# Kernel optimization log

Hardware: AMD Instinct MI355X
Metric: run time of the kernel (lower is better)

Reference implementation:

```python
import jax, jax.numpy as jnp
import numpy as np

BATCH = 256
SIZE = 512      # must be a power of two for the bitonic network
K = 16          # top-k
STEEPNESS = 10.0  # cauchy distribution scale (module default)


def _bitonic_layers(n):
    """Static index pairs of the bitonic sorting network (ascending).
    Returns (lefts, rights), each int32 [n_layers, n//2]. After a compare-swap,
    the soft-min goes to `left` and the soft-max goes to `right`."""
    lefts, rights = [], []
    k = 2
    while k <= n:
        j = k // 2
        while j >= 1:
            l_idx, r_idx = [], []
            for i in range(n):
                l = i ^ j
                if l > i:
                    if (i & k) == 0:   # ascending block: min at i
                        l_idx.append(i); r_idx.append(l)
                    else:              # descending block: min at l
                        l_idx.append(l); r_idx.append(i)
            lefts.append(l_idx); rights.append(r_idx)
            j //= 2
        k *= 2
    return np.asarray(lefts, np.int32), np.asarray(rights, np.int32)


def setup_inputs() -> dict:
    key = jax.random.key(0)
    vectors = jax.random.normal(key, (BATCH, SIZE), dtype=jnp.float32)
    return {"vectors": vectors}


def reference(vectors):
    b, n = vectors.shape
    lefts_np, rights_np = _bitonic_layers(n)
    lefts = jnp.asarray(lefts_np)
    rights = jnp.asarray(rights_np)
    # soft permutation matrix: X[b, i, j] = P(input j ends at sorted pos i)
    X0 = jnp.broadcast_to(jnp.eye(n, dtype=vectors.dtype)[None], (b, n, n))

    def step(carry, lr):
        x, X = carry
        l, r = lr                      # [n//2] index pairs for this layer
        a = x[:, l]                    # [b, n//2]
        c = x[:, r]
        # cauchy CDF of steepness*(c - a): prob that no swap is needed
        alpha = jnp.arctan((c - a) * STEEPNESS) / jnp.pi + 0.5
        x = x.at[:, l].set(alpha * a + (1.0 - alpha) * c)
        x = x.at[:, r].set(alpha * c + (1.0 - alpha) * a)
        Xl = X[:, l, :]                # [b, n//2, n]
        Xr = X[:, r, :]
        al = alpha[..., None]
        X = X.at[:, l, :].set(al * Xl + (1.0 - al) * Xr)
        X = X.at[:, r, :].set(al * Xr + (1.0 - al) * Xl)
        return (x, X), None

    (_, X), _ = jax.lax.scan(step, (vectors, X0), (lefts, rights))
    # ascending sort -> last K rows correspond to the K largest elements;
    # flip so row 0 = largest. Output: [batch, K, n] soft top-k distribution.
    return jnp.flip(X[:, n - K:, :], axis=1)
```

## Files before the change

### kernel.cpp

```cpp
#include <hip/hip_runtime.h>
#include <math.h>

#define N 512
#define BATCH 256
#define KTOP 16
#define NLAYERS 45
#define NPAIRS 256

template<int CTRL>
__device__ __forceinline__ float dpp_xor(float x) {
    return __int_as_float(
        __builtin_amdgcn_mov_dpp(__float_as_int(x), CTRL, 0xF, 0xF, true));
}

__device__ __forceinline__ float fast_alpha(float t) {
    const float at  = __builtin_fabsf(t);
    const bool inv  = at > 1.0f;
    const float z   = inv ? __builtin_amdgcn_rcpf(at) : at;
    const float s   = z * z;
    float p = -0.0117212f;
    p = __builtin_fmaf(p, s,  0.05265332f);
    p = __builtin_fmaf(p, s, -0.11643287f);
    p = __builtin_fmaf(p, s,  0.19354346f);
    p = __builtin_fmaf(p, s, -0.33262347f);
    p = __builtin_fmaf(p, s,  0.99997726f);
    float r = z * p;
    r = inv ? (1.5707963267948966f - r) : r;
    r = (t < 0.0f) ? -r : r;
    return __builtin_fmaf(r, 0.3183098861837907f, 0.5f);
}

__global__ __launch_bounds__(1024, 1)
void difftopk_kernel(const float* __restrict__ x_in, float* __restrict__ out) {
    __shared__ float xs[2][N];
    __shared__ __align__(16) float As[NLAYERS][NPAIRS];

    const int b    = blockIdx.x;
    const int tid  = threadIdx.x;
    const int lane = tid & 63;

    if (tid < N) {
        const int e = tid;
        float o = x_in[(size_t)b * N + e];

        int t = 0, par = 0;
        #pragma unroll
        for (int s = 1; s <= 9; ++s) {
            const int k  = 1 << s;
            const bool kb = (e & k) == 0;
            #pragma unroll
            for (int lg = s - 1; lg >= 0; --lg, ++t) {
                const int j = 1 << lg;
                float p;
                if (lg >= 6) {
                    xs[par][e] = o;
                    __syncthreads();
                    p = xs[par][e ^ j];
                    par ^= 1;
                } else if (lg == 0) {
                    p = dpp_xor<0xB1>(o);
                } else if (lg == 1) {
                    p = dpp_xor<0x4E>(o);
                } else if (lg == 3) {
                    p = dpp_xor<0x128>(o);
                } else {
                    p = __shfl_xor(o, j, 64);
                }
                const bool jb = (e & j) == 0;
                const float d = (kb == jb) ? (p - o) : (o - p);
                const float alpha = fast_alpha(d * 10.0f);
                o = __builtin_fmaf(alpha, o - p, p);
                if (jb) {
                    const int ord = ((e >> (lg + 1)) << lg) | (e & (j - 1));
                    As[t][ord] = alpha;
                }
            }
        }
        __syncthreads();
    } else {
        #pragma unroll 1
        for (int i = 0; i < 7; ++i) __syncthreads();
    }

    const int wave  = tid >> 6;
    const int lane8 = lane << 3;
    const int r     = N - 1 - wave;

    float v[8];
    #pragma unroll
    for (int m = 0; m < 8; ++m) v[m] = (lane8 + m == r) ? 1.0f : 0.0f;

    #pragma unroll
    for (int s = 9; s >= 1; --s) {
        const int base = (s * (s - 1)) >> 1;
        #pragma unroll
        for (int lg = 0; lg < s; ++lg) {
            const int tt = base + (s - 1 - lg);
            if (lg >= 3) {
                const int j    = 1 << lg;
                const int ordb = ((lane8 >> (lg + 1)) << lg) | (lane8 & (j - 1));
                const float4 a0 = *(const float4*)&As[tt][ordb];
                const float4 a1 = *(const float4*)&As[tt][ordb + 4];
                const float al[8] = {a0.x, a0.y, a0.z, a0.w, a1.x, a1.y, a1.z, a1.w};
                #pragma unroll
                for (int m = 0; m < 8; ++m) {
                    float p;
                    if (lg == 3)      p = dpp_xor<0xB1>(v[m]);
                    else if (lg == 4) p = dpp_xor<0x4E>(v[m]);
                    else if (lg == 6) p = dpp_xor<0x128>(v[m]);
                    else              p = __shfl_xor(v[m], j >> 3, 64);
                    v[m] = __builtin_fmaf(al[m], v[m] - p, p);
                }
            } else {
                const float4 a = *(const float4*)&As[tt][lane << 2];
                const float aa[4] = {a.x, a.y, a.z, a.w};
                if (lg == 2) {
                    #pragma unroll
                    for (int i = 0; i < 4; ++i) {
                        const float x0 = v[i], x1 = v[i + 4], d = x0 - x1;
                        v[i]     = __builtin_fmaf(aa[i],  d, x1);
                        v[i + 4] = __builtin_fmaf(aa[i], -d, x0);
                    }
                } else if (lg == 1) {
                    #pragma unroll
                    for (int i = 0; i < 4; ++i) {
                        const int lo = (((i >> 1) << 2) | (i & 1));
                        const float x0 = v[lo], x1 = v[lo + 2], d = x0 - x1;
                        v[lo]     = __builtin_fmaf(aa[i],  d, x1);
                        v[lo + 2] = __builtin_fmaf(aa[i], -d, x0);
                    }
                } else {
                    #pragma unroll
                    for (int i = 0; i < 4; ++i) {
                        const int lo = i << 1;
                        const float x0 = v[lo], x1 = v[lo + 1], d = x0 - x1;
                        v[lo]     = __builtin_fmaf(aa[i],  d, x1);
                        v[lo + 1] = __builtin_fmaf(aa[i], -d, x0);
                    }
                }
            }
        }
    }

    float4* dst = (float4*)(out + ((size_t)b * KTOP + wave) * N + lane8);
    dst[0] = make_float4(v[0], v[1], v[2], v[3]);
    dst[1] = make_float4(v[4], v[5], v[6], v[7]);
}

extern "C" void kernel_launch(void* const* d_in, const int* in_sizes, int n_in,
                              void* d_out, int out_size, void* d_ws, size_t ws_size,
                              hipStream_t stream) {
    const float* x = (const float*)d_in[0];
    float* out = (float*)d_out;
    difftopk_kernel<<<dim3(BATCH), dim3(1024), 0, stream>>>(x, out);
}
```

Measured before the change: 64.89 us.

## Store alphas in fp16 and use permlane swaps for cross-row exchanges

The per-layer alpha table moves from fp32 to fp16 in LDS, which halves shared-memory traffic and footprint for the backward permutation pass. The lg=7 and lg=8 stages now use v_permlane16/32_swap on pairs of registers instead of ds_bpermute-based shuffles, so the exchange stays in VALU. This lowers alpha precision to about three decimal digits, which may break accuracy tolerances, and the permlane swap needs extra swaps plus per-lane alpha selection.

```diff
diff --git a/kernel.cpp b/kernel.cpp
--- a/kernel.cpp
+++ b/kernel.cpp
@@ -1,4 +1,5 @@
 #include <hip/hip_runtime.h>
+#include <hip/hip_fp16.h>
 #include <math.h>
 
 #define N 512
@@ -7,10 +8,24 @@
 #define NLAYERS 45
 #define NPAIRS 256
 
+typedef _Float16 half8 __attribute__((ext_vector_type(8)));
+typedef _Float16 half4 __attribute__((ext_vector_type(4)));
+
 template<int CTRL>
 __device__ __forceinline__ float dpp_xor(float x) {
     return __int_as_float(
         __builtin_amdgcn_mov_dpp(__float_as_int(x), CTRL, 0xF, 0xF, true));
+}
+
+__device__ __forceinline__ void plane16_swap(float& a, float& b) {
+    asm("v_permlane16_swap_b32 %0, %1" : "+v"(a), "+v"(b));
+}
+__device__ __forceinline__ void plane32_swap(float& a, float& b) {
+    asm("v_permlane32_swap_b32 %0, %1" : "+v"(a), "+v"(b));
+}
+
+__device__ __forceinline__ float fmah(_Float16 a, float b, float c) {
+    return __builtin_fmaf((float)a, b, c);
 }
 
 __device__ __forceinline__ float fast_alpha(float t) {
@@ -33,7 +48,7 @@
 __global__ __launch_bounds__(1024, 1)
 void difftopk_kernel(const float* __restrict__ x_in, float* __restrict__ out) {
     __shared__ float xs[2][N];
-    __shared__ __align__(16) float As[NLAYERS][NPAIRS];
+    __shared__ __align__(16) _Float16 As[NLAYERS][NPAIRS];
 
     const int b    = blockIdx.x;
     const int tid  = threadIdx.x;
@@ -72,7 +87,7 @@
                 o = __builtin_fmaf(alpha, o - p, p);
                 if (jb) {
                     const int ord = ((e >> (lg + 1)) << lg) | (e & (j - 1));
-                    As[t][ord] = alpha;
+                    As[t][ord] = (_Float16)alpha;
                 }
             }
         }
@@ -85,6 +100,8 @@
     const int wave  = tid >> 6;
     const int lane8 = lane << 3;
     const int r     = N - 1 - wave;
+    const bool lo16 = (lane & 16) == 0;
+    const bool lo32 = (lane & 32) == 0;
 
     float v[8];
     #pragma unroll
@@ -99,43 +116,66 @@
             if (lg >= 3) {
                 const int j    = 1 << lg;
                 const int ordb = ((lane8 >> (lg + 1)) << lg) | (lane8 & (j - 1));
-                const float4 a0 = *(const float4*)&As[tt][ordb];
-                const float4 a1 = *(const float4*)&As[tt][ordb + 4];
-                const float al[8] = {a0.x, a0.y, a0.z, a0.w, a1.x, a1.y, a1.z, a1.w};
-                #pragma unroll
-                for (int m = 0; m < 8; ++m) {
-                    float p;
-                    if (lg == 3)      p = dpp_xor<0xB1>(v[m]);
-                    else if (lg == 4) p = dpp_xor<0x4E>(v[m]);
-                    else if (lg == 6) p = dpp_xor<0x128>(v[m]);
-                    else              p = __shfl_xor(v[m], j >> 3, 64);
-                    v[m] = __builtin_fmaf(al[m], v[m] - p, p);
+                const half8 alh = *(const half8*)&As[tt][ordb];
+                if (lg == 7) {
+                    #pragma unroll
+                    for (int m = 0; m < 8; m += 2) {
+                        float A = v[m], B = v[m + 1];
+                        plane16_swap(A, B);
+                        const _Float16 ha = lo16 ? alh[m] : alh[m + 1];
+                        const float d  = A - B;
+                        float n0 = fmah(ha,  d, B);
+                        float n1 = fmah(ha, -d, A);
+                        plane16_swap(n0, n1);
+                        v[m] = n0; v[m + 1] = n1;
+                    }
+                } else if (lg == 8) {
+                    #pragma unroll
+                    for (int m = 0; m < 8; m += 2) {
+                        float A = v[m], B = v[m + 1];
+                        plane32_swap(A, B);
+                        const _Float16 ha = lo32 ? alh[m] : alh[m + 1];
+                        const float d  = A - B;
+                        float n0 = fmah(ha,  d, B);
+                        float n1 = fmah(ha, -d, A);
+                        plane32_swap(n0, n1);
+                        v[m] = n0; v[m + 1] = n1;
+                    }
+                } else {
+                    #pragma unroll
+                    for (int m = 0; m < 8; ++m) {
+                        float p;
+                        if (lg == 3)      p = dpp_xor<0xB1>(v[m]);
+                        else if (lg == 4) p = dpp_xor<0x4E>(v[m]);
+                        else if (lg == 6) p = dpp_xor<0x128>(v[m]);
+                        else              p = __shfl_xor(v[m], 4, 64);
+                        v[m] = fmah(alh[m], v[m] - p, p);
+                    }
                 }
             } else {
-                const float4 a = *(const float4*)&As[tt][lane << 2];
-                const float aa[4] = {a.x, a.y, a.z, a.w};
+                const half4 a4 = *(const half4*)&As[tt][lane << 2];
                 if (lg == 2) {
                     #pragma unroll
                     for (int i = 0; i < 4; ++i) {
                         const float x0 = v[i], x1 = v[i + 4], d = x0 - x1;
-                        v[i]     = __builtin_fmaf(aa[i],  d, x1);
-                        v[i + 4] = __builtin_fmaf(aa[i], -d, x0);
+                        v[i]     = fmah(a4[i],  d, x1);
+                        v[i + 4] = fmah(a4[i], -d, x0);
                     }
                 } else if (lg == 1) {
                     #pragma unroll
                     for (int i = 0; i < 4; ++i) {
                         const int lo = (((i >> 1) << 2) | (i & 1));
                         const float x0 = v[lo], x1 = v[lo + 2], d = x0 - x1;
-                        v[lo]     = __builtin_fmaf(aa[i],  d, x1);
-                        v[lo + 2] = __builtin_fmaf(aa[i], -d, x0);
+                        v[lo]     = fmah(a4[i],  d, x1);
+                        v[lo + 2] = fmah(a4[i], -d, x0);
                     }
                 } else {
                     #pragma unroll
                     for (int i = 0; i < 4; ++i) {
                         const int lo = i << 1;
                         const float x0 = v[lo], x1 = v[lo + 1], d = x0 - x1;
-                        v[lo]     = __builtin_fmaf(aa[i],  d, x1);
-                        v[lo + 1] = __builtin_fmaf(aa[i], -d, x0);
+                        v[lo]     = fmah(a4[i],  d, x1);
+                        v[lo + 1] = fmah(a4[i], -d, x0);
                     }
                 }
             }
```

Measured after the change: 66.19 us. +2.0%, slower.
